# Performance work log

Measured on AMD Instinct MI355X. Metric: run time of the kernel, lower is better.

Reference implementation:

```python
import jax, jax.numpy as jnp
import numpy as np

HIDDEN_DIM = 128


def setup_inputs() -> dict:
    key = jax.random.key(0)
    ks = jax.random.split(key, 7)
    n_edges, edge_dim, edge_hidden, d = 20000, 16, 128, HIDDEN_DIM
    h_v = jax.random.normal(ks[0], (n_edges, d), dtype=jnp.float32)
    h_w = jax.random.normal(ks[1], (n_edges, d), dtype=jnp.float32)
    edge_features = jax.random.normal(ks[2], (n_edges, edge_dim), dtype=jnp.float32)
    W1 = jax.random.normal(ks[3], (edge_dim, edge_hidden), dtype=jnp.float32) * (1.0 / np.sqrt(edge_dim))
    b1 = jnp.zeros((edge_hidden,), dtype=jnp.float32)
    W2 = jax.random.normal(ks[4], (edge_hidden, d * d), dtype=jnp.float32) * (1.0 / np.sqrt(edge_hidden))
    b2 = jnp.zeros((d * d,), dtype=jnp.float32)
    return {"h_v": h_v, "h_w": h_w, "edge_features": edge_features,
            "W1": W1, "b1": b1, "W2": W2, "b2": b2}


def reference(h_v, h_w, edge_features, W1, b1, W2, b2):
    d = HIDDEN_DIM
    # Edge MLP: edge_dim -> edge_hidden -> d*d
    hidden = jax.nn.relu(edge_features @ W1 + b1)          # (E, edge_hidden)
    A = (hidden @ W2 + b2).reshape(-1, d, d)               # (E, d, d) per-edge matrices
    # Batched matrix-vector product: messages_e = A_e @ h_w_e
    messages = jnp.einsum('eij,ej->ei', A, h_w)            # (E, d)
    return messages
```

## Files before the change

### kernel.cpp

```cpp
#include <hip/hip_runtime.h>

#define E_EDGES 20000
#define D_DIM   128
#define NBA     136
#define SLAB_B  21504

typedef _Float16 f16x8 __attribute__((ext_vector_type(8)));
typedef _Float16 f16x4 __attribute__((ext_vector_type(4)));
typedef _Float16 f16x2 __attribute__((ext_vector_type(2)));
typedef float    floatx4 __attribute__((ext_vector_type(4)));

union F8 { f16x8 v; f16x2 h2[4]; unsigned int u[4]; };
union F4 { f16x4 v; f16x2 h2[2]; unsigned int u[2]; };

__device__ __forceinline__ unsigned short f32_to_f16(float f) {
    _Float16 h = (_Float16)f;
    return __builtin_bit_cast(unsigned short, h);
}

__global__ __launch_bounds__(256) void prep_w2(
    const float* __restrict__ W2, const float* __restrict__ b2,
    uint4* __restrict__ bpf)
{
    __shared__ __align__(16) unsigned short tile[17408];
    const int h = blockIdx.x;
    const int t = threadIdx.x;

    if (h < 129) {
        const float* src = (h < 128) ? (W2 + (size_t)h * (D_DIM * D_DIM)) : b2;
        #pragma unroll
        for (int r = 0; r < 16; ++r) {
            const float4 v = ((const float4*)src)[r * 256 + t];
            int c   = (r * 256 + t) * 4;
            int col = c >> 7;
            int k   = c & 127;
            unsigned int u0 = f32_to_f16(v.x) | ((unsigned int)f32_to_f16(v.y) << 16);
            unsigned int u1 = f32_to_f16(v.z) | ((unsigned int)f32_to_f16(v.w) << 16);
            *(uint2*)&tile[col * 136 + k] = make_uint2(u0, u1);
        }
        __syncthreads();
        #pragma unroll
        for (int r2 = 0; r2 < 8; ++r2) {
            int cidx = r2 * 256 + t;
            int ll = cidx & 63;
            int nt = (cidx >> 6) & 1;
            int jq = (cidx >> 7) & 3;
            int ch = (cidx >> 9) & 3;
            int col = 32 * ch + 16 * nt + (ll & 15);
            int k0  = 32 * jq + 8 * (ll >> 4);
            bpf[(size_t)h * 2048 + cidx] = *(const uint4*)&tile[col * 136 + k0];
        }
    } else {
        #pragma unroll
        for (int r2 = 0; r2 < 8; ++r2)
            bpf[(size_t)h * 2048 + r2 * 256 + t] = make_uint4(0, 0, 0, 0);
    }
}

__global__ __launch_bounds__(256, 3)
void edge_main(const uint4* __restrict__ bpf, const float* __restrict__ hw,
               const float* __restrict__ ef, const float* __restrict__ W1,
               const float* __restrict__ b1, float* __restrict__ out)
{
    __shared__ __align__(16) char slab[SLAB_B];
    const int bx  = blockIdx.x;
    const int ch  = bx & 3;
    const int eg  = bx >> 2;
    const int tid = threadIdx.x;
    const int jq  = tid >> 6;
    const int l   = tid & 63;
    const int l4  = l >> 4;
    const int lm  = l & 15;
    const int e0  = eg * 80;

    F8 hws[5];
    #pragma unroll
    for (int m = 0; m < 5; ++m) {
        const float* ph = hw + (size_t)(e0 + 16 * m + lm) * 128 + 32 * jq + 8 * l4;
        const float4 x = *(const float4*)ph;
        const float4 y = *(const float4*)(ph + 4);
        hws[m].h2[0] = (f16x2){(_Float16)x.x, (_Float16)x.y};
        hws[m].h2[1] = (f16x2){(_Float16)x.z, (_Float16)x.w};
        hws[m].h2[2] = (f16x2){(_Float16)y.x, (_Float16)y.y};
        hws[m].h2[3] = (f16x2){(_Float16)y.z, (_Float16)y.w};
    }

    {
        F4 A[5];
        #pragma unroll
        for (int m = 0; m < 5; ++m) {
            const float4 q4 = *(const float4*)(ef + (size_t)(e0 + 16 * m + lm) * 16 + 4 * l4);
            A[m].h2[0] = (f16x2){(_Float16)q4.x, (_Float16)q4.y};
            A[m].h2[1] = (f16x2){(_Float16)q4.z, (_Float16)q4.w};
        }
        F4 Bw[2];
        float bv[2];
        #pragma unroll
        for (int nn = 0; nn < 2; ++nn) {
            const int col = jq * 32 + nn * 16 + lm;
            float w0 = W1[(4 * l4 + 0) * 128 + col];
            float w1 = W1[(4 * l4 + 1) * 128 + col];
            float w2 = W1[(4 * l4 + 2) * 128 + col];
            float w3 = W1[(4 * l4 + 3) * 128 + col];
            Bw[nn].h2[0] = (f16x2){(_Float16)w0, (_Float16)w1};
            Bw[nn].h2[1] = (f16x2){(_Float16)w2, (_Float16)w3};
            bv[nn] = b1[col];
        }
        #pragma unroll
        for (int m = 0; m < 5; ++m) {
            floatx4 H0 = (floatx4){bv[0], bv[0], bv[0], bv[0]};
            floatx4 H1 = (floatx4){bv[1], bv[1], bv[1], bv[1]};
            H0 = __builtin_amdgcn_mfma_f32_16x16x16f16(A[m].v, Bw[0].v, H0, 0, 0, 0);
            H1 = __builtin_amdgcn_mfma_f32_16x16x16f16(A[m].v, Bw[1].v, H1, 0, 0, 0);
            #pragma unroll
            for (int r = 0; r < 4; ++r) {
                const int e = 16 * m + 4 * l4 + r;
                *(unsigned short*)(slab + e * 264 + (jq * 32 + lm) * 2) =
                    f32_to_f16(fmaxf(H0[r], 0.f));
                *(unsigned short*)(slab + e * 264 + (jq * 32 + 16 + lm) * 2) =
                    f32_to_f16(fmaxf(H1[r], 0.f));
            }
        }
        if (tid < 80) {
            *(unsigned int*)(slab + tid * 264 + 256) = 0x00003C00u;
            *(unsigned int*)(slab + tid * 264 + 260) = 0u;
        }
    }

    floatx4 C[5][2];
    #pragma unroll
    for (int m = 0; m < 5; ++m)
        #pragma unroll
        for (int nt = 0; nt < 2; ++nt)
            C[m][nt] = (floatx4){0.f, 0.f, 0.f, 0.f};

    const f16x8* bpf8 = (const f16x8*)bpf;
    const int cbase = ch * 512 + jq * 128 + l;

    f16x8 B[4][2];
    auto loadB = [&](int h, f16x8 (&Bq)[2]) {
        const f16x8* p = bpf8 + (size_t)h * 2048 + cbase;
        Bq[0] = p[0];
        Bq[1] = p[64];
    };
    loadB(0, B[0]);
    loadB(1, B[1]);
    loadB(2, B[2]);
    loadB(3, B[3]);

    __syncthreads();

    auto doH = [&](int h, const uint2 (&hid)[5]) {
        const int hh = h & 3;
        #pragma unroll
        for (int m = 0; m < 5; ++m) {
            unsigned int s   = (hh < 2) ? hid[m].x : hid[m].y;
            unsigned int sel = (hh & 1) ? 0x03020302u : 0x01000100u;
            f16x2 d = __builtin_bit_cast(f16x2, __builtin_amdgcn_perm(0u, s, sel));
            F8 a;
            #pragma unroll
            for (int i = 0; i < 4; ++i) a.h2[i] = hws[m].h2[i] * d;
            C[m][0] = __builtin_amdgcn_mfma_f32_16x16x32_f16(a.v, B[hh][0], C[m][0], 0, 0, 0);
            C[m][1] = __builtin_amdgcn_mfma_f32_16x16x32_f16(a.v, B[hh][1], C[m][1], 0, 0, 0);
        }
        loadB(h + 4, B[hh]);
    };
    auto readHid = [&](int q, uint2 (&hid)[5]) {
        #pragma unroll
        for (int m = 0; m < 5; ++m)
            hid[m] = *(const uint2*)(slab + (16 * m + lm) * 264 + q * 8);
    };

    uint2 hid0[5], hid1[5];
    readHid(0, hid0);
    #pragma unroll 1
    for (int q = 0; q < 32; q += 2) {
        readHid(q + 1, hid1);
        doH(4 * q + 0, hid0);
        doH(4 * q + 1, hid0);
        doH(4 * q + 2, hid0);
        doH(4 * q + 3, hid0);
        readHid(q + 2, hid0);
        doH(4 * q + 4, hid1);
        doH(4 * q + 5, hid1);
        doH(4 * q + 6, hid1);
        doH(4 * q + 7, hid1);
    }
    doH(128, hid0);
    doH(129, hid0);
    doH(130, hid0);
    doH(131, hid0);

    float* red = (float*)slab;
    #pragma unroll 1
    for (int src = 1; src < 4; ++src) {
        __syncthreads();
        if (jq == src) {
            #pragma unroll
            for (int m = 0; m < 5; ++m)
                #pragma unroll
                for (int nt = 0; nt < 2; ++nt)
                    #pragma unroll
                    for (int r = 0; r < 4; ++r)
                        red[((m * 2 + nt) * 4 + r) * 64 + l] = C[m][nt][r];
        }
        __syncthreads();
        if (jq == 0) {
            #pragma unroll
            for (int m = 0; m < 5; ++m)
                #pragma unroll
                for (int nt = 0; nt < 2; ++nt)
                    #pragma unroll
                    for (int r = 0; r < 4; ++r)
                        C[m][nt][r] += red[((m * 2 + nt) * 4 + r) * 64 + l];
        }
    }
    if (jq == 0) {
        #pragma unroll
        for (int m = 0; m < 5; ++m)
            #pragma unroll
            for (int nt = 0; nt < 2; ++nt)
                #pragma unroll
                for (int r = 0; r < 4; ++r)
                    out[(size_t)(e0 + 16 * m + 4 * l4 + r) * D_DIM
                        + 32 * ch + 16 * nt + lm] = C[m][nt][r];
    }
}

extern "C" void kernel_launch(void* const* d_in, const int* in_sizes, int n_in,
                              void* d_out, int out_size, void* d_ws, size_t ws_size,
                              hipStream_t stream) {
    const float* h_w = (const float*)d_in[1];
    const float* ef  = (const float*)d_in[2];
    const float* W1  = (const float*)d_in[3];
    const float* b1  = (const float*)d_in[4];
    const float* W2  = (const float*)d_in[5];
    const float* b2  = (const float*)d_in[6];
    float* out = (float*)d_out;

    uint4* bpf = (uint4*)d_ws;

    hipLaunchKernelGGL(prep_w2, dim3(NBA), dim3(256), 0, stream, W2, b2, bpf);
    hipLaunchKernelGGL(edge_main, dim3(1000), dim3(256), 0, stream,
                       bpf, h_w, ef, W1, b1, out);
}
```

Before: 158.3 us.

## Split hidden reduction into thirds with persistent atomic work queue

The main kernel becomes persistent: 768 blocks pull work items from a global atomic counter. Each item covers 80 edges, one output column chunk and one third of the 132 hidden rows, and partial results are accumulated into a zeroed output with float atomics. h_w is converted to fp16 once in the prep kernel instead of inside each block. The goal is better load balance and shorter per-block tails across CUs. The cost is three times the layer-1 MLP recomputation, extra memsets, atomic traffic on the output, and nondeterministic summation order.

New measurement: 182.4 us. 15.2% more time.

```diff
diff --git a/kernel.cpp b/kernel.cpp
--- a/kernel.cpp
+++ b/kernel.cpp
@@ -3,7 +3,9 @@
 #define E_EDGES 20000
 #define D_DIM   128
 #define NBA     136
+#define NBC     184
 #define SLAB_B  21504
+#define N_ITEMS 3000
 
 typedef _Float16 f16x8 __attribute__((ext_vector_type(8)));
 typedef _Float16 f16x4 __attribute__((ext_vector_type(4)));
@@ -18,212 +20,237 @@
     return __builtin_bit_cast(unsigned short, h);
 }
 
-__global__ __launch_bounds__(256) void prep_w2(
+__global__ __launch_bounds__(256) void prep_all(
     const float* __restrict__ W2, const float* __restrict__ b2,
-    uint4* __restrict__ bpf)
+    const float* __restrict__ hw,
+    uint4* __restrict__ bpf, unsigned short* __restrict__ hwb)
 {
     __shared__ __align__(16) unsigned short tile[17408];
-    const int h = blockIdx.x;
-    const int t = threadIdx.x;
-
-    if (h < 129) {
-        const float* src = (h < 128) ? (W2 + (size_t)h * (D_DIM * D_DIM)) : b2;
-        #pragma unroll
-        for (int r = 0; r < 16; ++r) {
-            const float4 v = ((const float4*)src)[r * 256 + t];
-            int c   = (r * 256 + t) * 4;
-            int col = c >> 7;
-            int k   = c & 127;
-            unsigned int u0 = f32_to_f16(v.x) | ((unsigned int)f32_to_f16(v.y) << 16);
-            unsigned int u1 = f32_to_f16(v.z) | ((unsigned int)f32_to_f16(v.w) << 16);
-            *(uint2*)&tile[col * 136 + k] = make_uint2(u0, u1);
-        }
-        __syncthreads();
-        #pragma unroll
-        for (int r2 = 0; r2 < 8; ++r2) {
-            int cidx = r2 * 256 + t;
-            int ll = cidx & 63;
-            int nt = (cidx >> 6) & 1;
-            int jq = (cidx >> 7) & 3;
-            int ch = (cidx >> 9) & 3;
-            int col = 32 * ch + 16 * nt + (ll & 15);
-            int k0  = 32 * jq + 8 * (ll >> 4);
-            bpf[(size_t)h * 2048 + cidx] = *(const uint4*)&tile[col * 136 + k0];
+    const int bx = blockIdx.x;
+    const int t  = threadIdx.x;
+
+    if (bx < NBA) {
+        const int h = bx;
+        if (h < 129) {
+            const float* src = (h < 128) ? (W2 + (size_t)h * (D_DIM * D_DIM)) : b2;
+            #pragma unroll
+            for (int r = 0; r < 16; ++r) {
+                const float4 v = ((const float4*)src)[r * 256 + t];
+                int c   = (r * 256 + t) * 4;
+                int col = c >> 7;
+                int k   = c & 127;
+                unsigned int u0 = f32_to_f16(v.x) | ((unsigned int)f32_to_f16(v.y) << 16);
+                unsigned int u1 = f32_to_f16(v.z) | ((unsigned int)f32_to_f16(v.w) << 16);
+                *(uint2*)&tile[col * 136 + k] = make_uint2(u0, u1);
+            }
+            __syncthreads();
+            #pragma unroll
+            for (int r2 = 0; r2 < 8; ++r2) {
+                int cidx = r2 * 256 + t;
+                int ll = cidx & 63;
+                int nt = (cidx >> 6) & 1;
+                int jq = (cidx >> 7) & 3;
+                int ch = (cidx >> 9) & 3;
+                int col = 32 * ch + 16 * nt + (ll & 15);
+                int k0  = 32 * jq + 8 * (ll >> 4);
+                bpf[(size_t)h * 2048 + cidx] = *(const uint4*)&tile[col * 136 + k0];
+            }
+        } else {
+            #pragma unroll
+            for (int r2 = 0; r2 < 8; ++r2)
+                bpf[(size_t)h * 2048 + r2 * 256 + t] = make_uint4(0, 0, 0, 0);
         }
     } else {
-        #pragma unroll
-        for (int r2 = 0; r2 < 8; ++r2)
-            bpf[(size_t)h * 2048 + r2 * 256 + t] = make_uint4(0, 0, 0, 0);
+        int i0 = (bx - NBA) * 256 + t;
+        for (int i = i0; i < (E_EDGES * D_DIM) / 4; i += NBC * 256) {
+            const float4 v = ((const float4*)hw)[i];
+            union { unsigned short u16[4]; uint2 u2; } o;
+            o.u16[0] = f32_to_f16(v.x);
+            o.u16[1] = f32_to_f16(v.y);
+            o.u16[2] = f32_to_f16(v.z);
+            o.u16[3] = f32_to_f16(v.w);
+            ((uint2*)hwb)[i] = o.u2;
+        }
     }
 }
 
 __global__ __launch_bounds__(256, 3)
-void edge_main(const uint4* __restrict__ bpf, const float* __restrict__ hw,
+void edge_main(const uint4* __restrict__ bpf, const uint4* __restrict__ hwb,
                const float* __restrict__ ef, const float* __restrict__ W1,
-               const float* __restrict__ b1, float* __restrict__ out)
+               const float* __restrict__ b1, float* __restrict__ out,
+               int* __restrict__ counter)
 {
     __shared__ __align__(16) char slab[SLAB_B];
-    const int bx  = blockIdx.x;
-    const int ch  = bx & 3;
-    const int eg  = bx >> 2;
+    __shared__ int s_id;
     const int tid = threadIdx.x;
     const int jq  = tid >> 6;
     const int l   = tid & 63;
     const int l4  = l >> 4;
     const int lm  = l & 15;
-    const int e0  = eg * 80;
-
-    F8 hws[5];
-    #pragma unroll
-    for (int m = 0; m < 5; ++m) {
-        const float* ph = hw + (size_t)(e0 + 16 * m + lm) * 128 + 32 * jq + 8 * l4;
-        const float4 x = *(const float4*)ph;
-        const float4 y = *(const float4*)(ph + 4);
-        hws[m].h2[0] = (f16x2){(_Float16)x.x, (_Float16)x.y};
-        hws[m].h2[1] = (f16x2){(_Float16)x.z, (_Float16)x.w};
-        hws[m].h2[2] = (f16x2){(_Float16)y.x, (_Float16)y.y};
-        hws[m].h2[3] = (f16x2){(_Float16)y.z, (_Float16)y.w};
-    }
-
-    {
-        F4 A[5];
-        #pragma unroll
-        for (int m = 0; m < 5; ++m) {
-            const float4 q4 = *(const float4*)(ef + (size_t)(e0 + 16 * m + lm) * 16 + 4 * l4);
-            A[m].h2[0] = (f16x2){(_Float16)q4.x, (_Float16)q4.y};
-            A[m].h2[1] = (f16x2){(_Float16)q4.z, (_Float16)q4.w};
-        }
-        F4 Bw[2];
-        float bv[2];
-        #pragma unroll
-        for (int nn = 0; nn < 2; ++nn) {
-            const int col = jq * 32 + nn * 16 + lm;
-            float w0 = W1[(4 * l4 + 0) * 128 + col];
-            float w1 = W1[(4 * l4 + 1) * 128 + col];
-            float w2 = W1[(4 * l4 + 2) * 128 + col];
-            float w3 = W1[(4 * l4 + 3) * 128 + col];
-            Bw[nn].h2[0] = (f16x2){(_Float16)w0, (_Float16)w1};
-            Bw[nn].h2[1] = (f16x2){(_Float16)w2, (_Float16)w3};
-            bv[nn] = b1[col];
-        }
-        #pragma unroll
-        for (int m = 0; m < 5; ++m) {
-            floatx4 H0 = (floatx4){bv[0], bv[0], bv[0], bv[0]};
-            floatx4 H1 = (floatx4){bv[1], bv[1], bv[1], bv[1]};
-            H0 = __builtin_amdgcn_mfma_f32_16x16x16f16(A[m].v, Bw[0].v, H0, 0, 0, 0);
-            H1 = __builtin_amdgcn_mfma_f32_16x16x16f16(A[m].v, Bw[1].v, H1, 0, 0, 0);
-            #pragma unroll
-            for (int r = 0; r < 4; ++r) {
-                const int e = 16 * m + 4 * l4 + r;
-                *(unsigned short*)(slab + e * 264 + (jq * 32 + lm) * 2) =
-                    f32_to_f16(fmaxf(H0[r], 0.f));
-                *(unsigned short*)(slab + e * 264 + (jq * 32 + 16 + lm) * 2) =
-                    f32_to_f16(fmaxf(H1[r], 0.f));
-            }
-        }
-        if (tid < 80) {
-            *(unsigned int*)(slab + tid * 264 + 256) = 0x00003C00u;
-            *(unsigned int*)(slab + tid * 264 + 260) = 0u;
-        }
-    }
-
-    floatx4 C[5][2];
-    #pragma unroll
-    for (int m = 0; m < 5; ++m)
-        #pragma unroll
-        for (int nt = 0; nt < 2; ++nt)
-            C[m][nt] = (floatx4){0.f, 0.f, 0.f, 0.f};
-
     const f16x8* bpf8 = (const f16x8*)bpf;
-    const int cbase = ch * 512 + jq * 128 + l;
-
-    f16x8 B[4][2];
-    auto loadB = [&](int h, f16x8 (&Bq)[2]) {
-        const f16x8* p = bpf8 + (size_t)h * 2048 + cbase;
-        Bq[0] = p[0];
-        Bq[1] = p[64];
-    };
-    loadB(0, B[0]);
-    loadB(1, B[1]);
-    loadB(2, B[2]);
-    loadB(3, B[3]);
-
-    __syncthreads();
-
-    auto doH = [&](int h, const uint2 (&hid)[5]) {
-        const int hh = h & 3;
-        #pragma unroll
-        for (int m = 0; m < 5; ++m) {
-            unsigned int s   = (hh < 2) ? hid[m].x : hid[m].y;
-            unsigned int sel = (hh & 1) ? 0x03020302u : 0x01000100u;
-            f16x2 d = __builtin_bit_cast(f16x2, __builtin_amdgcn_perm(0u, s, sel));
-            F8 a;
-            #pragma unroll
-            for (int i = 0; i < 4; ++i) a.h2[i] = hws[m].h2[i] * d;
-            C[m][0] = __builtin_amdgcn_mfma_f32_16x16x32_f16(a.v, B[hh][0], C[m][0], 0, 0, 0);
-            C[m][1] = __builtin_amdgcn_mfma_f32_16x16x32_f16(a.v, B[hh][1], C[m][1], 0, 0, 0);
-        }
-        loadB(h + 4, B[hh]);
-    };
-    auto readHid = [&](int q, uint2 (&hid)[5]) {
+
+    for (;;) {
+        __syncthreads();
+        if (tid == 0) s_id = atomicAdd(counter, 1);
+        __syncthreads();
+        const int id = s_id;
+        if (id >= N_ITEMS) break;
+
+        const int third = id / 1000;
+        const int r1    = id - third * 1000;
+        const int ch    = r1 / 250;
+        const int eg    = r1 - ch * 250;
+        const int e0    = eg * 80;
+        const int qs    = third * 11;
+        const int cbase = ch * 512 + jq * 128 + l;
+
+        F8 hws[5];
         #pragma unroll
         for (int m = 0; m < 5; ++m)
-            hid[m] = *(const uint2*)(slab + (16 * m + lm) * 264 + q * 8);
-    };
-
-    uint2 hid0[5], hid1[5];
-    readHid(0, hid0);
-    #pragma unroll 1
-    for (int q = 0; q < 32; q += 2) {
-        readHid(q + 1, hid1);
-        doH(4 * q + 0, hid0);
-        doH(4 * q + 1, hid0);
-        doH(4 * q + 2, hid0);
-        doH(4 * q + 3, hid0);
-        readHid(q + 2, hid0);
-        doH(4 * q + 4, hid1);
-        doH(4 * q + 5, hid1);
-        doH(4 * q + 6, hid1);
-        doH(4 * q + 7, hid1);
-    }
-    doH(128, hid0);
-    doH(129, hid0);
-    doH(130, hid0);
-    doH(131, hid0);
-
-    float* red = (float*)slab;
-    #pragma unroll 1
-    for (int src = 1; src < 4; ++src) {
+            hws[m].v = ((const F8*)hwb)[(e0 + 16 * m + lm) * 16 + 4 * jq + l4].v;
+
+        f16x8 B[4][2];
+        auto loadB = [&](int h, f16x8 (&Bq)[2]) {
+            const f16x8* p = bpf8 + (size_t)h * 2048 + cbase;
+            Bq[0] = p[0];
+            Bq[1] = p[64];
+        };
+        const int h0 = 4 * qs;
+        loadB(h0 + 0, B[0]);
+        loadB(h0 + 1, B[1]);
+        loadB(h0 + 2, B[2]);
+        loadB(h0 + 3, B[3]);
+
+        {
+            F4 A[5];
+            #pragma unroll
+            for (int m = 0; m < 5; ++m) {
+                const float4 q4 = *(const float4*)(ef + (size_t)(e0 + 16 * m + lm) * 16 + 4 * l4);
+                A[m].h2[0] = (f16x2){(_Float16)q4.x, (_Float16)q4.y};
+                A[m].h2[1] = (f16x2){(_Float16)q4.z, (_Float16)q4.w};
+            }
+            F4 Bw[2];
+            float bv[2];
+            #pragma unroll
+            for (int nn = 0; nn < 2; ++nn) {
+                const int col = jq * 32 + nn * 16 + lm;
+                float w0 = W1[(4 * l4 + 0) * 128 + col];
+                float w1 = W1[(4 * l4 + 1) * 128 + col];
+                float w2 = W1[(4 * l4 + 2) * 128 + col];
+                float w3 = W1[(4 * l4 + 3) * 128 + col];
+                Bw[nn].h2[0] = (f16x2){(_Float16)w0, (_Float16)w1};
+                Bw[nn].h2[1] = (f16x2){(_Float16)w2, (_Float16)w3};
+                bv[nn] = b1[col];
+            }
+            #pragma unroll
+            for (int m = 0; m < 5; ++m) {
+                floatx4 H0 = (floatx4){bv[0], bv[0], bv[0], bv[0]};
+                floatx4 H1 = (floatx4){bv[1], bv[1], bv[1], bv[1]};
+                H0 = __builtin_amdgcn_mfma_f32_16x16x16f16(A[m].v, Bw[0].v, H0, 0, 0, 0);
+                H1 = __builtin_amdgcn_mfma_f32_16x16x16f16(A[m].v, Bw[1].v, H1, 0, 0, 0);
+                #pragma unroll
+                for (int r = 0; r < 4; ++r) {
+                    const int e = 16 * m + 4 * l4 + r;
+                    *(unsigned short*)(slab + e * 264 + (jq * 32 + lm) * 2) =
+                        f32_to_f16(fmaxf(H0[r], 0.f));
+                    *(unsigned short*)(slab + e * 264 + (jq * 32 + 16 + lm) * 2) =
+                        f32_to_f16(fmaxf(H1[r], 0.f));
+                }
+            }
+            if (tid < 80) {
+                *(unsigned int*)(slab + tid * 264 + 256) = 0x00003C00u;
+                *(unsigned int*)(slab + tid * 264 + 260) = 0u;
+            }
+        }
+
+        floatx4 C[5][2];
+        #pragma unroll
+        for (int m = 0; m < 5; ++m)
+            #pragma unroll
+            for (int nt = 0; nt < 2; ++nt)
+                C[m][nt] = (floatx4){0.f, 0.f, 0.f, 0.f};
+
         __syncthreads();
-        if (jq == src) {
+
+        auto doH = [&](int h, const uint2 (&hid)[5]) {
+            const int hh = h & 3;
+            #pragma unroll
+            for (int m = 0; m < 5; ++m) {
+                unsigned int s   = (hh < 2) ? hid[m].x : hid[m].y;
+                unsigned int sel = (hh & 1) ? 0x03020302u : 0x01000100u;
+                f16x2 d = __builtin_bit_cast(f16x2, __builtin_amdgcn_perm(0u, s, sel));
+                F8 a;
+                #pragma unroll
+                for (int i = 0; i < 4; ++i) a.h2[i] = hws[m].h2[i] * d;
+                C[m][0] = __builtin_amdgcn_mfma_f32_16x16x32_f16(a.v, B[hh][0], C[m][0], 0, 0, 0);
+                C[m][1] = __builtin_amdgcn_mfma_f32_16x16x32_f16(a.v, B[hh][1], C[m][1], 0, 0, 0);
+            }
+            loadB(h + 4, B[hh]);
+        };
+        auto readHid = [&](int q, uint2 (&hid)[5]) {
+            #pragma unroll
+            for (int m = 0; m < 5; ++m)
+                hid[m] = *(const uint2*)(slab + (16 * m + lm) * 264 + q * 8);
+        };
+
+        uint2 hid0[5], hid1[5];
+        readHid(qs, hid0);
+        #pragma unroll 1
+        for (int q = qs; q + 2 < qs + 11; q += 2) {
+            readHid(q + 1, hid1);
+            doH(4 * q + 0, hid0);
+            doH(4 * q + 1, hid0);
+            doH(4 * q + 2, hid0);
+            doH(4 * q + 3, hid0);
+            readHid(q + 2, hid0);
+            doH(4 * q + 4, hid1);
+            doH(4 * q + 5, hid1);
+            doH(4 * q + 6, hid1);
+            doH(4 * q + 7, hid1);
+        }
+        {
+            const int qT = qs + 10;
+            doH(4 * qT + 0, hid0);
+            doH(4 * qT + 1, hid0);
+            doH(4 * qT + 2, hid0);
+            doH(4 * qT + 3, hid0);
+        }
+
+        float* red = (float*)slab;
+        #pragma unroll 1
+        for (int src = 1; src < 4; ++src) {
+            __syncthreads();
+            if (jq == src) {
+                #pragma unroll
+                for (int m = 0; m < 5; ++m)
+                    #pragma unroll
+                    for (int nt = 0; nt < 2; ++nt)
+                        #pragma unroll
+                        for (int r = 0; r < 4; ++r)
+                            red[((m * 2 + nt) * 4 + r) * 64 + l] = C[m][nt][r];
+            }
+            __syncthreads();
+            if (jq == 0) {
+                #pragma unroll
+                for (int m = 0; m < 5; ++m)
+                    #pragma unroll
+                    for (int nt = 0; nt < 2; ++nt)
+                        #pragma unroll
+                        for (int r = 0; r < 4; ++r)
+                            C[m][nt][r] += red[((m * 2 + nt) * 4 + r) * 64 + l];
+            }
+        }
+        if (jq == 0) {
             #pragma unroll
             for (int m = 0; m < 5; ++m)
                 #pragma unroll
                 for (int nt = 0; nt < 2; ++nt)
                     #pragma unroll
                     for (int r = 0; r < 4; ++r)
-                        red[((m * 2 + nt) * 4 + r) * 64 + l] = C[m][nt][r];
-        }
-        __syncthreads();
-        if (jq == 0) {
-            #pragma unroll
-            for (int m = 0; m < 5; ++m)
-                #pragma unroll
-                for (int nt = 0; nt < 2; ++nt)
-                    #pragma unroll
-                    for (int r = 0; r < 4; ++r)
-                        C[m][nt][r] += red[((m * 2 + nt) * 4 + r) * 64 + l];
-        }
-    }
-    if (jq == 0) {
-        #pragma unroll
-        for (int m = 0; m < 5; ++m)
-            #pragma unroll
-            for (int nt = 0; nt < 2; ++nt)
-                #pragma unroll
-                for (int r = 0; r < 4; ++r)
-                    out[(size_t)(e0 + 16 * m + 4 * l4 + r) * D_DIM
-                        + 32 * ch + 16 * nt + lm] = C[m][nt][r];
+                        unsafeAtomicAdd(out + (size_t)(e0 + 16 * m + 4 * l4 + r) * D_DIM
+                                            + 32 * ch + 16 * nt + lm,
+                                        C[m][nt][r]);
+        }
     }
 }
 
@@ -238,9 +265,15 @@
     const float* b2  = (const float*)d_in[6];
     float* out = (float*)d_out;
 
-    uint4* bpf = (uint4*)d_ws;
-
-    hipLaunchKernelGGL(prep_w2, dim3(NBA), dim3(256), 0, stream, W2, b2, bpf);
-    hipLaunchKernelGGL(edge_main, dim3(1000), dim3(256), 0, stream,
-                       bpf, h_w, ef, W1, b1, out);
-}
+    char* ws = (char*)d_ws;
+    uint4*          bpf     = (uint4*)ws;
+    unsigned short* hwb     = (unsigned short*)(ws + 4456448);
+    int*            counter = (int*)(ws + 4456448 + 5120000);
+
+    (void)hipMemsetAsync(out, 0, (size_t)E_EDGES * D_DIM * sizeof(float), stream);
+    (void)hipMemsetAsync(counter, 0, sizeof(int), stream);
+    hipLaunchKernelGGL(prep_all, dim3(NBA + NBC), dim3(256), 0, stream,
+                       W2, b2, h_w, bpf, hwb);
+    hipLaunchKernelGGL(edge_main, dim3(768), dim3(256), 0, stream,
+                       bpf, (const uint4*)hwb, ef, W1, b1, out, counter);
+}
```
